# Optimization experiments

Hardware: AMD Instinct MI355X
Metric: run time of the kernel (lower is better)

The kernel has to match this reference:

```python
import jax, jax.numpy as jnp
import numpy as np

B, C, H, W = 32, 256, 32, 32
HID, NPATH = 128, 4


def setup_inputs() -> dict:
    key = jax.random.key(0)
    ks = jax.random.split(key, 16)
    s = lambda *sh: 1.0 / np.sqrt(sh[-1])
    inp = {
        "lidar": jax.random.normal(ks[0], (B, C, H, W), jnp.float32),
        "hsi": jax.random.normal(ks[1], (B, C, H, W), jnp.float32),
        "x": jax.random.normal(ks[2], (B, C, H, W), jnp.float32),
        # shared Cross_Self_attention params
        "Wq": jax.random.normal(ks[3], (C, C), jnp.float32) * s(C, C),
        "bq": jnp.zeros((C,), jnp.float32),
        "Wk": jax.random.normal(ks[4], (C, C), jnp.float32) * s(C, C),
        "bk": jnp.zeros((C,), jnp.float32),
        "Wv": jax.random.normal(ks[5], (C, C), jnp.float32) * s(C, C),
        "bv": jnp.zeros((C,), jnp.float32),
        # 1x1 conv: [out=C, in=2C]
        "conv_w": jax.random.normal(ks[6], (C, 2 * C), jnp.float32) * s(C, 2 * C),
        "conv_b": jnp.zeros((C,), jnp.float32),
        # router MLP
        "r_w1": jax.random.normal(ks[7], (HID, 2 * C), jnp.float32) * s(HID, 2 * C),
        "r_b1": jnp.zeros((HID,), jnp.float32),
        "r_w2": jax.random.normal(ks[8], (NPATH, HID), jnp.float32) * s(NPATH, HID),
        "r_b2": jnp.zeros((NPATH,), jnp.float32),
    }
    return inp


def _cross_self_attn(xq, yv, Wq, bq, Wk, bk, Wv, bv):
    # xq, yv: [b, s, c]
    q = xq @ Wq.T + bq
    k = xq @ Wk.T + bk
    v = yv @ Wv.T + bv
    probs = jax.nn.softmax(jnp.einsum("bsc,btc->bst", q, k), axis=-1)  # [b,s,s]
    return jnp.einsum("bst,btc->bsc", probs, q * v)  # bilinear value Q*V


def reference(lidar, hsi, x, Wq, bq, Wk, bk, Wv, bv, conv_w, conv_b, r_w1, r_b1, r_w2, r_b2):
    b, c, h, w = lidar.shape
    # Router: concat channels, spatial mean pool, MLP, sigmoid
    g = jnp.concatenate([lidar, hsi], axis=1).mean(axis=(2, 3))  # [b, 2c]
    path_prob = jax.nn.sigmoid(jax.nn.relu(g @ r_w1.T + r_b1) @ r_w2.T + r_b2)

    l = lidar.reshape(b, c, h * w).transpose(0, 2, 1)  # b (h w) c
    hh = hsi.reshape(b, c, h * w).transpose(0, 2, 1)

    h_emb = _cross_self_attn(l, hh, Wq, bq, Wk, bk, Wv, bv)  # [b, hw, c]
    l_emb = _cross_self_attn(hh, l, Wq, bq, Wk, bk, Wv, bv)

    h_emb = h_emb.transpose(0, 2, 1).reshape(b, c, h, w)
    l_emb = l_emb.transpose(0, 2, 1).reshape(b, c, h, w)

    cat = jnp.concatenate([l_emb, h_emb], axis=1)  # [b, 2c, h, w]
    emb = jnp.einsum("bihw,oi->bohw", cat, conv_w) + conv_b[None, :, None, None] + x
    return emb, path_prob
```

## Files before the change

### kernel.cpp

```cpp
#include <hip/hip_runtime.h>
#include <stdint.h>

typedef unsigned short u16;
typedef unsigned int u32;
typedef _Float16 f16;
typedef _Float16 f16x8 __attribute__((ext_vector_type(8)));
typedef _Float16 f16x4 __attribute__((ext_vector_type(4)));
typedef float f32x4 __attribute__((ext_vector_type(4)));

#define B_ 32
#define C_ 256
#define S_ 1024

__global__ __launch_bounds__(256) void k_mlp(
    const float* __restrict__ g,
    const float* __restrict__ w1, const float* __restrict__ b1,
    const float* __restrict__ w2, const float* __restrict__ b2,
    float* __restrict__ out)
{
    int b = blockIdx.x, tid = threadIdx.x;
    __shared__ float sg[512];
    __shared__ float sh[128];
    sg[tid]     = g[b*512 + tid]       * (1.0f/1024.0f);
    sg[tid+256] = g[b*512 + 256 + tid] * (1.0f/1024.0f);
    __syncthreads();
    if (tid < 128){
        float a = b1[tid];
        const float* w = w1 + (size_t)tid*512;
        #pragma unroll 4
        for (int k = 0; k < 512; k += 4){
            float4 wv = *(const float4*)(w + k);
            a += sg[k]*wv.x + sg[k+1]*wv.y + sg[k+2]*wv.z + sg[k+3]*wv.w;
        }
        sh[tid] = fmaxf(a, 0.f);
    }
    __syncthreads();
    if (tid < 4){
        float a = b2[tid];
        const float* w = w2 + (size_t)tid*128;
        for (int k = 0; k < 128; ++k) a += sh[k]*w[k];
        out[(size_t)8388608 + b*4 + tid] = 1.f/(1.f+expf(-a));
    }
}

__global__ __launch_bounds__(256) void k_cvtw(
    const float* __restrict__ Wq, const float* __restrict__ Wk,
    const float* __restrict__ Wv, const float* __restrict__ cw,
    f16* __restrict__ Wqf, f16* __restrict__ Wkf,
    f16* __restrict__ Wvf, f16* __restrict__ cwf)
{
    int i = (blockIdx.x*256 + threadIdx.x) * 4;
    const float* src; f16* dst; int off;
    if (i < 65536){ src = Wq; dst = Wqf; off = i; }
    else if (i < 131072){ src = Wk; dst = Wkf; off = i - 65536; }
    else if (i < 196608){ src = Wv; dst = Wvf; off = i - 131072; }
    else { src = cw; dst = cwf; off = i - 196608; }
    float4 v = *(const float4*)(src + off);
    f16x4 r = { (f16)v.x, (f16)v.y, (f16)v.z, (f16)v.w };
    *(f16x4*)(dst + off) = r;
}

__global__ __launch_bounds__(256) void k_cvt(
    const float* __restrict__ lidar, const float* __restrict__ hsi,
    f16* __restrict__ lidT, f16* __restrict__ hsiT,
    float* __restrict__ g)
{
    int z = blockIdx.z, which = z >> 5, b = z & 31;
    const float* src = (which ? hsi : lidar) + (size_t)b*C_*S_;
    f16* dst = (which ? hsiT : lidT) + (size_t)b*S_*C_;
    int tid = threadIdx.x;
    int c4 = blockIdx.y*64 + (tid&15)*4;
    int s4 = blockIdx.x*64 + (tid>>4)*4;
    float4 m[4];
    #pragma unroll
    for (int r = 0; r < 4; ++r) m[r] = *(const float4*)(src + (size_t)(c4+r)*S_ + s4);
    f16x4 t0 = { (f16)m[0].x, (f16)m[1].x, (f16)m[2].x, (f16)m[3].x };
    f16x4 t1 = { (f16)m[0].y, (f16)m[1].y, (f16)m[2].y, (f16)m[3].y };
    f16x4 t2 = { (f16)m[0].z, (f16)m[1].z, (f16)m[2].z, (f16)m[3].z };
    f16x4 t3 = { (f16)m[0].w, (f16)m[1].w, (f16)m[2].w, (f16)m[3].w };
    *(f16x4*)(dst + (size_t)(s4+0)*C_ + c4) = t0;
    *(f16x4*)(dst + (size_t)(s4+1)*C_ + c4) = t1;
    *(f16x4*)(dst + (size_t)(s4+2)*C_ + c4) = t2;
    *(f16x4*)(dst + (size_t)(s4+3)*C_ + c4) = t3;
    float ps[4];
    #pragma unroll
    for (int r = 0; r < 4; ++r){
        ps[r] = m[r].x + m[r].y + m[r].z + m[r].w;
        ps[r] += __shfl_xor(ps[r], 16, 64);
        ps[r] += __shfl_xor(ps[r], 32, 64);
    }
    __shared__ float sred[4][64];
    int wv = tid>>6, lane = tid&63;
    if ((lane>>4) == 0){
        #pragma unroll
        for (int r = 0; r < 4; ++r) sred[wv][(lane&15)*4 + r] = ps[r];
    }
    __syncthreads();
    if (tid < 64){
        float v = sred[0][tid] + sred[1][tid] + sred[2][tid] + sred[3][tid];
        atomicAdd(&g[b*512 + which*256 + blockIdx.y*64 + tid], v);
    }
}

__global__ __launch_bounds__(256) void k_qkv(
    const f16* __restrict__ lidT, const f16* __restrict__ hsiT,
    const f16* __restrict__ Wqf, const f16* __restrict__ Wkf, const f16* __restrict__ Wvf,
    const float* __restrict__ bq, const float* __restrict__ bk, const float* __restrict__ bv,
    f16* __restrict__ Qf_l, f16* __restrict__ Kf_l,
    f16* __restrict__ Qf_h, f16* __restrict__ Kf_h,
    f16* __restrict__ Qt_l, f16* __restrict__ Qt_h,
    f16* __restrict__ Vt_l, f16* __restrict__ Vt_h)
{
    int z = blockIdx.z, combo = z >> 5, b = z & 31, ww = combo % 3;
    const f16* In = ((combo < 3) ? lidT : hsiT) + (size_t)b*S_*C_;
    const f16* Wf = (ww==0) ? Wqf : (ww==1) ? Wkf : Wvf;
    const float* bias = (ww==0) ? bq : (ww==1) ? bk : bv;
    int s0 = blockIdx.x*64, o0 = blockIdx.y*64;
    int tid = threadIdx.x, w = tid>>6, lane = tid&63, quad = lane>>4, l15 = lane&15;

    __shared__ __align__(16) f16 sA[64*72];
    __shared__ __align__(16) f16 sB[64*72];

    f32x4 D[4];
    #pragma unroll
    for (int i = 0; i < 4; ++i) D[i] = (f32x4){0.f,0.f,0.f,0.f};

    int row = tid>>2, c16 = (tid&3)*16;
    for (int c0 = 0; c0 < 256; c0 += 64){
        __syncthreads();
        *(f16x8*)&sA[row*72 + c16]     = *(const f16x8*)(In + (size_t)(s0+row)*C_ + c0 + c16);
        *(f16x8*)&sA[row*72 + c16 + 8] = *(const f16x8*)(In + (size_t)(s0+row)*C_ + c0 + c16 + 8);
        *(f16x8*)&sB[row*72 + c16]     = *(const f16x8*)(Wf + (size_t)(o0+row)*C_ + c0 + c16);
        *(f16x8*)&sB[row*72 + c16 + 8] = *(const f16x8*)(Wf + (size_t)(o0+row)*C_ + c0 + c16 + 8);
        __syncthreads();
        #pragma unroll
        for (int sub = 0; sub < 2; ++sub){
            f16x8 a = *(const f16x8*)&sA[(w*16+l15)*72 + sub*32 + quad*8];
            #pragma unroll
            for (int bt = 0; bt < 4; ++bt){
                f16x8 bb = *(const f16x8*)&sB[(bt*16+l15)*72 + sub*32 + quad*8];
                D[bt] = __builtin_amdgcn_mfma_f32_16x16x32_f16(a, bb, D[bt], 0,0,0);
            }
        }
    }
    float bi[4];
    #pragma unroll
    for (int bt = 0; bt < 4; ++bt) bi[bt] = bias[o0 + bt*16 + l15];

    if (ww == 0){
        f16* F = ((combo==0) ? Qf_l : Qf_h) + (size_t)b*S_*C_;
        #pragma unroll
        for (int bt = 0; bt < 4; ++bt)
            #pragma unroll
            for (int r = 0; r < 4; ++r)
                F[(size_t)(s0 + w*16 + quad*4 + r)*C_ + o0 + bt*16 + l15] = (f16)(D[bt][r] + bi[bt]);
    } else if (ww == 1){
        f16* F = ((combo==1) ? Kf_l : Kf_h) + (size_t)b*S_*C_;
        #pragma unroll
        for (int bt = 0; bt < 4; ++bt)
            #pragma unroll
            for (int r = 0; r < 4; ++r)
                F[(size_t)(s0 + w*16 + quad*4 + r)*C_ + o0 + bt*16 + l15] = (f16)(D[bt][r] + bi[bt]);
    }
    if (ww != 1){
        __syncthreads();
        #pragma unroll
        for (int bt = 0; bt < 4; ++bt)
            #pragma unroll
            for (int r = 0; r < 4; ++r)
                sA[(bt*16+l15)*72 + w*16 + quad*4 + r] = (f16)(D[bt][r] + bi[bt]);
        __syncthreads();
        f16* T = (combo==0) ? Qt_l : (combo==3) ? Qt_h : (combo==2) ? Vt_l : Vt_h;
        T += (size_t)b*C_*S_;
        int o_r = tid>>2, s16b = (tid&3)*16;
        *(f16x8*)(T + (size_t)(o0+o_r)*S_ + s0 + s16b)     = *(const f16x8*)&sA[o_r*72 + s16b];
        *(f16x8*)(T + (size_t)(o0+o_r)*S_ + s0 + s16b + 8) = *(const f16x8*)&sA[o_r*72 + s16b + 8];
    }
}

__global__ __launch_bounds__(256) void k_qv(
    const f16* __restrict__ Qt_l, const f16* __restrict__ Qt_h,
    const f16* __restrict__ Vt_l, const f16* __restrict__ Vt_h,
    f16* __restrict__ QVT1, f16* __restrict__ QVT2)
{
    size_t idx = (size_t)(blockIdx.x*256 + threadIdx.x) * 8;
    f16x8 a = *(const f16x8*)(Qt_l+idx);
    f16x8 b = *(const f16x8*)(Vt_h+idx);
    *(f16x8*)(QVT1+idx) = a*b;
    f16x8 c = *(const f16x8*)(Qt_h+idx);
    f16x8 d = *(const f16x8*)(Vt_l+idx);
    *(f16x8*)(QVT2+idx) = c*d;
}

__global__ __launch_bounds__(256, 2) void k_attn(
    const f16* __restrict__ Qf_l, const f16* __restrict__ Kf_l,
    const f16* __restrict__ Qf_h, const f16* __restrict__ Kf_h,
    const f16* __restrict__ QVT1, const f16* __restrict__ QVT2,
    f16* __restrict__ cat)
{
    int inst = blockIdx.y;
    int b = inst >> 1, which = inst & 1;
    const f16* Qf  = (which ? Qf_h : Qf_l) + (size_t)b*S_*C_;
    const f16* Kf  = (which ? Kf_h : Kf_l) + (size_t)b*S_*C_;
    const f16* QVT = (which ? QVT2 : QVT1) + (size_t)b*C_*S_;
    f16* outp = cat + (size_t)b*S_*512 + (which ? 0 : 256);
    int s0 = blockIdx.x*64;
    int tid = threadIdx.x, w = tid>>6, lane = tid&63, quad = lane>>4, l15 = lane&15;

    __shared__ __align__(16) f16 sK[64*264];
    __shared__ __align__(16) f16 sV[256*72];
    __shared__ __align__(16) f16 sPw[4][16*66];

    f16x8 qa[8];
    {
        const f16* qrow = Qf + (size_t)(s0 + w*16 + l15)*C_ + quad*8;
        #pragma unroll
        for (int i = 0; i < 8; ++i) qa[i] = *(const f16x8*)(qrow + i*32);
    }
    float mrun[4], lpart[4];
    #pragma unroll
    for (int r = 0; r < 4; ++r){ mrun[r] = -1e30f; lpart[r] = 0.f; }
    f32x4 pacc[16];
    #pragma unroll
    for (int i = 0; i < 16; ++i) pacc[i] = (f32x4){0.f,0.f,0.f,0.f};

    f16x8 kreg[8], vreg[8];
    #pragma unroll
    for (int p = 0; p < 8; ++p){
        int idx = p*256 + tid;
        kreg[p] = *(const f16x8*)(Kf + (size_t)(idx>>5)*C_ + (idx&31)*8);
        vreg[p] = *(const f16x8*)(QVT + (size_t)(idx>>3)*S_ + (idx&7)*8);
    }

    for (int tt = 0; tt < 16; ++tt){
        __syncthreads();
        #pragma unroll
        for (int p = 0; p < 8; ++p){
            int idx = p*256 + tid;
            *(f16x8*)&sK[(idx>>5)*264 + (idx&31)*8] = kreg[p];
            *(f16x8*)&sV[(idx>>3)*72  + (idx&7)*8]  = vreg[p];
        }
        __syncthreads();

        if (tt < 15){
            int t0n = (tt+1)*64;
            #pragma unroll
            for (int p = 0; p < 8; ++p){
                int idx = p*256 + tid;
                kreg[p] = *(const f16x8*)(Kf + (size_t)(t0n + (idx>>5))*C_ + (idx&31)*8);
                vreg[p] = *(const f16x8*)(QVT + (size_t)(idx>>3)*S_ + t0n + (idx&7)*8);
            }
        }

        f32x4 sacc[4];
        #pragma unroll
        for (int bt = 0; bt < 4; ++bt) sacc[bt] = (f32x4){0.f,0.f,0.f,0.f};
        __builtin_amdgcn_s_setprio(1);
        #pragma unroll
        for (int ks = 0; ks < 8; ++ks){
            #pragma unroll
            for (int bt = 0; bt < 4; ++bt){
                f16x8 kb = *(const f16x8*)&sK[(bt*16+l15)*264 + ks*32 + quad*8];
                sacc[bt] = __builtin_amdgcn_mfma_f32_16x16x32_f16(qa[ks], kb, sacc[bt], 0,0,0);
            }
        }
        __builtin_amdgcn_s_setprio(0);

        float tm[4];
        #pragma unroll
        for (int r = 0; r < 4; ++r){
            float t = fmaxf(fmaxf(sacc[0][r], sacc[1][r]), fmaxf(sacc[2][r], sacc[3][r]));
            #pragma unroll
            for (int off = 1; off < 16; off <<= 1) t = fmaxf(t, __shfl_xor(t, off, 64));
            tm[r] = t;
        }
        bool need = (tm[0] > mrun[0]+8.f) | (tm[1] > mrun[1]+8.f) |
                    (tm[2] > mrun[2]+8.f) | (tm[3] > mrun[3]+8.f);
        if (__any(need)){
            #pragma unroll
            for (int r = 0; r < 4; ++r){
                float mn = fmaxf(mrun[r], tm[r]);
                float al = __expf(mrun[r] - mn);
                mrun[r] = mn;
                lpart[r] *= al;
                #pragma unroll
                for (int cf = 0; cf < 16; ++cf) pacc[cf][r] *= al;
            }
        }
        #pragma unroll
        for (int r = 0; r < 4; ++r){
            float local = 0.f;
            #pragma unroll
            for (int bt = 0; bt < 4; ++bt){
                float p = __expf(sacc[bt][r] - mrun[r]);
                sPw[w][(quad*4+r)*66 + bt*16 + l15] = (f16)p;
                local += p;
            }
            lpart[r] += local;
        }
        f16x8 pa0 = *(const f16x8*)&sPw[w][l15*66 + quad*8];
        f16x8 pa1 = *(const f16x8*)&sPw[w][l15*66 + 32 + quad*8];

        __builtin_amdgcn_s_setprio(1);
        #pragma unroll
        for (int cf = 0; cf < 16; ++cf){
            f16x8 vb0 = *(const f16x8*)&sV[(cf*16+l15)*72 + quad*8];
            f16x8 vb1 = *(const f16x8*)&sV[(cf*16+l15)*72 + 32 + quad*8];
            pacc[cf] = __builtin_amdgcn_mfma_f32_16x16x32_f16(pa0, vb0, pacc[cf], 0,0,0);
            pacc[cf] = __builtin_amdgcn_mfma_f32_16x16x32_f16(pa1, vb1, pacc[cf], 0,0,0);
        }
        __builtin_amdgcn_s_setprio(0);
    }

    #pragma unroll
    for (int r = 0; r < 4; ++r){
        #pragma unroll
        for (int off = 1; off < 16; off <<= 1) lpart[r] += __shfl_xor(lpart[r], off, 64);
    }
    #pragma unroll
    for (int r = 0; r < 4; ++r){
        int s = w*16 + quad*4 + r;
        float rl = 1.f / lpart[r];
        #pragma unroll
        for (int cf = 0; cf < 16; ++cf)
            outp[(size_t)(s0+s)*512 + cf*16 + l15] = (f16)(pacc[cf][r] * rl);
    }
}

__global__ __launch_bounds__(256) void k_conv(
    const f16* __restrict__ cat, const f16* __restrict__ cwf,
    const float* __restrict__ cb, const float* __restrict__ x,
    float* __restrict__ out)
{
    int b = blockIdx.z;
    int s0 = blockIdx.x*64, o0 = blockIdx.y*64;
    int tid = threadIdx.x, w = tid>>6, lane = tid&63, quad = lane>>4, l15 = lane&15;

    __shared__ __align__(16) f16 sA[64*72];
    __shared__ __align__(16) f16 sB[64*72];

    f32x4 D[4];
    #pragma unroll
    for (int i = 0; i < 4; ++i) D[i] = (f32x4){0.f,0.f,0.f,0.f};

    const f16* catb = cat + (size_t)b*S_*512;
    int row = tid>>2, c16 = (tid&3)*16;
    for (int i0 = 0; i0 < 512; i0 += 64){
        __syncthreads();
        *(f16x8*)&sA[row*72 + c16]     = *(const f16x8*)(cwf + (size_t)(o0+row)*512 + i0 + c16);
        *(f16x8*)&sA[row*72 + c16 + 8] = *(const f16x8*)(cwf + (size_t)(o0+row)*512 + i0 + c16 + 8);
        *(f16x8*)&sB[row*72 + c16]     = *(const f16x8*)(catb + (size_t)(s0+row)*512 + i0 + c16);
        *(f16x8*)&sB[row*72 + c16 + 8] = *(const f16x8*)(catb + (size_t)(s0+row)*512 + i0 + c16 + 8);
        __syncthreads();
        #pragma unroll
        for (int sub = 0; sub < 2; ++sub){
            f16x8 a = *(const f16x8*)&sA[(w*16+l15)*72 + sub*32 + quad*8];
            #pragma unroll
            for (int bt = 0; bt < 4; ++bt){
                f16x8 bb = *(const f16x8*)&sB[(bt*16+l15)*72 + sub*32 + quad*8];
                D[bt] = __builtin_amdgcn_mfma_f32_16x16x32_f16(a, bb, D[bt], 0,0,0);
            }
        }
    }
    #pragma unroll
    for (int r = 0; r < 4; ++r){
        int o_loc = w*16 + quad*4 + r;
        float cbv = cb[o0 + o_loc];
        size_t base = (size_t)b*C_*S_ + (size_t)(o0+o_loc)*S_ + s0;
        #pragma unroll
        for (int bt = 0; bt < 4; ++bt){
            size_t a = base + bt*16 + l15;
            out[a] = D[bt][r] + cbv + x[a];
        }
    }
}

extern "C" void kernel_launch(void* const* d_in, const int* in_sizes, int n_in,
                              void* d_out, int out_size, void* d_ws, size_t ws_size,
                              hipStream_t stream)
{
    const float* lidar = (const float*)d_in[0];
    const float* hsi   = (const float*)d_in[1];
    const float* x     = (const float*)d_in[2];
    const float* Wq = (const float*)d_in[3];  const float* bq = (const float*)d_in[4];
    const float* Wk = (const float*)d_in[5];  const float* bk = (const float*)d_in[6];
    const float* Wv = (const float*)d_in[7];  const float* bv = (const float*)d_in[8];
    const float* cw = (const float*)d_in[9];  const float* cb = (const float*)d_in[10];
    const float* rw1 = (const float*)d_in[11]; const float* rb1 = (const float*)d_in[12];
    const float* rw2 = (const float*)d_in[13]; const float* rb2 = (const float*)d_in[14];
    float* outF = (float*)d_out;
    char* ws = (char*)d_ws;
    const size_t M = 1ull<<20;

    f16* lidT = (f16*)(ws +   0*M);
    f16* hsiT = (f16*)(ws +  16*M);
    f16* Qf_l = (f16*)(ws +  32*M);
    f16* Kf_l = (f16*)(ws +  48*M);
    f16* Qf_h = (f16*)(ws +  64*M);
    f16* Kf_h = (f16*)(ws +  80*M);
    f16* Qt_l = (f16*)(ws +  96*M);
    f16* Qt_h = (f16*)(ws + 112*M);
    f16* cat  = (f16*)(ws + 128*M);
    float* g  = (float*)(ws + 160*M);
    f16* Wqf  = (f16*)(ws + 161*M);
    f16* Wkf  = (f16*)(ws + 161*M + 131072);
    f16* Wvf  = (f16*)(ws + 161*M + 262144);
    f16* cwf  = (f16*)(ws + 161*M + 393216);
    f16* QVT1 = lidT;
    f16* QVT2 = hsiT;
    f16* Vt_l = (f16*)d_out;
    f16* Vt_h = (f16*)d_out + 8388608;

    hipMemsetAsync(g, 0, 4096*sizeof(float), stream);
    k_cvtw<<<320, 256, 0, stream>>>(Wq, Wk, Wv, cw, Wqf, Wkf, Wvf, cwf);
    k_cvt<<<dim3(16,4,64), 256, 0, stream>>>(lidar, hsi, lidT, hsiT, g);
    k_mlp<<<32, 256, 0, stream>>>(g, rw1, rb1, rw2, rb2, outF);
    k_qkv<<<dim3(16,4,192), 256, 0, stream>>>(lidT, hsiT, Wqf, Wkf, Wvf, bq, bk, bv,
                                              Qf_l, Kf_l, Qf_h, Kf_h, Qt_l, Qt_h, Vt_l, Vt_h);
    k_qv<<<4096, 256, 0, stream>>>(Qt_l, Qt_h, Vt_l, Vt_h, QVT1, QVT2);
    k_attn<<<dim3(16,64), 256, 0, stream>>>(Qf_l, Kf_l, Qf_h, Kf_h, QVT1, QVT2, cat);
    k_conv<<<dim3(16,4,32), 256, 0, stream>>>(cat, cwf, cb, x, outF);
}
```

Baseline: 400.9 us.

## Process two query tiles per attention block to reuse K/V shared tiles

Each attention block now handles 128 query rows (two 64-row groups per wave) instead of 64, so every K and QV tile staged in shared memory feeds twice as many MFMAs. This halves the block count and the total global K/V traffic. The register-prefetch double buffering of the next K/V tile is removed, and loads now go straight from global to shared memory between barriers. Register pressure roughly doubles for the accumulators (pacc now holds 32 f32x4 per thread), which risks spills or lower occupancy under launch_bounds(256,2). Load latency is also no longer hidden by prefetch.

```diff
diff --git a/kernel.cpp b/kernel.cpp
--- a/kernel.cpp
+++ b/kernel.cpp
@@ -204,126 +204,133 @@
     const f16* Kf  = (which ? Kf_h : Kf_l) + (size_t)b*S_*C_;
     const f16* QVT = (which ? QVT2 : QVT1) + (size_t)b*C_*S_;
     f16* outp = cat + (size_t)b*S_*512 + (which ? 0 : 256);
-    int s0 = blockIdx.x*64;
+    int s0 = blockIdx.x*128;
     int tid = threadIdx.x, w = tid>>6, lane = tid&63, quad = lane>>4, l15 = lane&15;
 
     __shared__ __align__(16) f16 sK[64*264];
     __shared__ __align__(16) f16 sV[256*72];
     __shared__ __align__(16) f16 sPw[4][16*66];
 
-    f16x8 qa[8];
-    {
-        const f16* qrow = Qf + (size_t)(s0 + w*16 + l15)*C_ + quad*8;
-        #pragma unroll
-        for (int i = 0; i < 8; ++i) qa[i] = *(const f16x8*)(qrow + i*32);
-    }
-    float mrun[4], lpart[4];
-    #pragma unroll
-    for (int r = 0; r < 4; ++r){ mrun[r] = -1e30f; lpart[r] = 0.f; }
-    f32x4 pacc[16];
-    #pragma unroll
-    for (int i = 0; i < 16; ++i) pacc[i] = (f32x4){0.f,0.f,0.f,0.f};
-
-    f16x8 kreg[8], vreg[8];
-    #pragma unroll
-    for (int p = 0; p < 8; ++p){
-        int idx = p*256 + tid;
-        kreg[p] = *(const f16x8*)(Kf + (size_t)(idx>>5)*C_ + (idx&31)*8);
-        vreg[p] = *(const f16x8*)(QVT + (size_t)(idx>>3)*S_ + (idx&7)*8);
-    }
+    f16x8 qa[2][8];
+    #pragma unroll
+    for (int g = 0; g < 2; ++g){
+        const f16* qrow = Qf + (size_t)(s0 + g*64 + w*16 + l15)*C_ + quad*8;
+        #pragma unroll
+        for (int i = 0; i < 8; ++i) qa[g][i] = *(const f16x8*)(qrow + i*32);
+    }
+    float mrun[2][4], lpart[2][4];
+    #pragma unroll
+    for (int g = 0; g < 2; ++g)
+        #pragma unroll
+        for (int r = 0; r < 4; ++r){ mrun[g][r] = -1e30f; lpart[g][r] = 0.f; }
+    f32x4 pacc[2][16];
+    #pragma unroll
+    for (int g = 0; g < 2; ++g)
+        #pragma unroll
+        for (int i = 0; i < 16; ++i) pacc[g][i] = (f32x4){0.f,0.f,0.f,0.f};
 
     for (int tt = 0; tt < 16; ++tt){
+        int t0 = tt*64;
         __syncthreads();
         #pragma unroll
         for (int p = 0; p < 8; ++p){
             int idx = p*256 + tid;
-            *(f16x8*)&sK[(idx>>5)*264 + (idx&31)*8] = kreg[p];
-            *(f16x8*)&sV[(idx>>3)*72  + (idx&7)*8]  = vreg[p];
-        }
-        __syncthreads();
-
-        if (tt < 15){
-            int t0n = (tt+1)*64;
-            #pragma unroll
-            for (int p = 0; p < 8; ++p){
-                int idx = p*256 + tid;
-                kreg[p] = *(const f16x8*)(Kf + (size_t)(t0n + (idx>>5))*C_ + (idx&31)*8);
-                vreg[p] = *(const f16x8*)(QVT + (size_t)(idx>>3)*S_ + t0n + (idx&7)*8);
-            }
-        }
-
-        f32x4 sacc[4];
-        #pragma unroll
-        for (int bt = 0; bt < 4; ++bt) sacc[bt] = (f32x4){0.f,0.f,0.f,0.f};
+            int row = idx >> 5, c8 = (idx & 31)*8;
+            *(f16x8*)&sK[row*264 + c8] = *(const f16x8*)(Kf + (size_t)(t0+row)*C_ + c8);
+        }
+        #pragma unroll
+        for (int p = 0; p < 8; ++p){
+            int idx = p*256 + tid;
+            int row = idx >> 3, t8 = (idx & 7)*8;
+            *(f16x8*)&sV[row*72 + t8] = *(const f16x8*)(QVT + (size_t)row*S_ + t0 + t8);
+        }
+        __syncthreads();
+
+        f32x4 sacc[2][4];
+        #pragma unroll
+        for (int g = 0; g < 2; ++g)
+            #pragma unroll
+            for (int bt = 0; bt < 4; ++bt) sacc[g][bt] = (f32x4){0.f,0.f,0.f,0.f};
         __builtin_amdgcn_s_setprio(1);
         #pragma unroll
         for (int ks = 0; ks < 8; ++ks){
             #pragma unroll
             for (int bt = 0; bt < 4; ++bt){
                 f16x8 kb = *(const f16x8*)&sK[(bt*16+l15)*264 + ks*32 + quad*8];
-                sacc[bt] = __builtin_amdgcn_mfma_f32_16x16x32_f16(qa[ks], kb, sacc[bt], 0,0,0);
+                sacc[0][bt] = __builtin_amdgcn_mfma_f32_16x16x32_f16(qa[0][ks], kb, sacc[0][bt], 0,0,0);
+                sacc[1][bt] = __builtin_amdgcn_mfma_f32_16x16x32_f16(qa[1][ks], kb, sacc[1][bt], 0,0,0);
             }
         }
         __builtin_amdgcn_s_setprio(0);
 
-        float tm[4];
-        #pragma unroll
-        for (int r = 0; r < 4; ++r){
-            float t = fmaxf(fmaxf(sacc[0][r], sacc[1][r]), fmaxf(sacc[2][r], sacc[3][r]));
-            #pragma unroll
-            for (int off = 1; off < 16; off <<= 1) t = fmaxf(t, __shfl_xor(t, off, 64));
-            tm[r] = t;
-        }
-        bool need = (tm[0] > mrun[0]+8.f) | (tm[1] > mrun[1]+8.f) |
-                    (tm[2] > mrun[2]+8.f) | (tm[3] > mrun[3]+8.f);
-        if (__any(need)){
+        f16x8 pa[2][2];
+        #pragma unroll
+        for (int g = 0; g < 2; ++g){
+            float tm[4];
             #pragma unroll
             for (int r = 0; r < 4; ++r){
-                float mn = fmaxf(mrun[r], tm[r]);
-                float al = __expf(mrun[r] - mn);
-                mrun[r] = mn;
-                lpart[r] *= al;
+                float t = fmaxf(fmaxf(sacc[g][0][r], sacc[g][1][r]),
+                                fmaxf(sacc[g][2][r], sacc[g][3][r]));
                 #pragma unroll
-                for (int cf = 0; cf < 16; ++cf) pacc[cf][r] *= al;
-            }
-        }
-        #pragma unroll
-        for (int r = 0; r < 4; ++r){
-            float local = 0.f;
-            #pragma unroll
-            for (int bt = 0; bt < 4; ++bt){
-                float p = __expf(sacc[bt][r] - mrun[r]);
-                sPw[w][(quad*4+r)*66 + bt*16 + l15] = (f16)p;
-                local += p;
-            }
-            lpart[r] += local;
-        }
-        f16x8 pa0 = *(const f16x8*)&sPw[w][l15*66 + quad*8];
-        f16x8 pa1 = *(const f16x8*)&sPw[w][l15*66 + 32 + quad*8];
+                for (int off = 1; off < 16; off <<= 1) t = fmaxf(t, __shfl_xor(t, off, 64));
+                tm[r] = t;
+            }
+            bool need = (tm[0] > mrun[g][0]+8.f) | (tm[1] > mrun[g][1]+8.f) |
+                        (tm[2] > mrun[g][2]+8.f) | (tm[3] > mrun[g][3]+8.f);
+            if (__any(need)){
+                #pragma unroll
+                for (int r = 0; r < 4; ++r){
+                    float mn = fmaxf(mrun[g][r], tm[r]);
+                    float al = __expf(mrun[g][r] - mn);
+                    mrun[g][r] = mn;
+                    lpart[g][r] *= al;
+                    #pragma unroll
+                    for (int cf = 0; cf < 16; ++cf) pacc[g][cf][r] *= al;
+                }
+            }
+            #pragma unroll
+            for (int r = 0; r < 4; ++r){
+                float local = 0.f;
+                #pragma unroll
+                for (int bt = 0; bt < 4; ++bt){
+                    float p = __expf(sacc[g][bt][r] - mrun[g][r]);
+                    sPw[w][(quad*4+r)*66 + bt*16 + l15] = (f16)p;
+                    local += p;
+                }
+                lpart[g][r] += local;
+            }
+            pa[g][0] = *(const f16x8*)&sPw[w][l15*66 + quad*8];
+            pa[g][1] = *(const f16x8*)&sPw[w][l15*66 + 32 + quad*8];
+        }
 
         __builtin_amdgcn_s_setprio(1);
         #pragma unroll
         for (int cf = 0; cf < 16; ++cf){
             f16x8 vb0 = *(const f16x8*)&sV[(cf*16+l15)*72 + quad*8];
             f16x8 vb1 = *(const f16x8*)&sV[(cf*16+l15)*72 + 32 + quad*8];
-            pacc[cf] = __builtin_amdgcn_mfma_f32_16x16x32_f16(pa0, vb0, pacc[cf], 0,0,0);
-            pacc[cf] = __builtin_amdgcn_mfma_f32_16x16x32_f16(pa1, vb1, pacc[cf], 0,0,0);
+            pacc[0][cf] = __builtin_amdgcn_mfma_f32_16x16x32_f16(pa[0][0], vb0, pacc[0][cf], 0,0,0);
+            pacc[0][cf] = __builtin_amdgcn_mfma_f32_16x16x32_f16(pa[0][1], vb1, pacc[0][cf], 0,0,0);
+            pacc[1][cf] = __builtin_amdgcn_mfma_f32_16x16x32_f16(pa[1][0], vb0, pacc[1][cf], 0,0,0);
+            pacc[1][cf] = __builtin_amdgcn_mfma_f32_16x16x32_f16(pa[1][1], vb1, pacc[1][cf], 0,0,0);
         }
         __builtin_amdgcn_s_setprio(0);
     }
 
     #pragma unroll
-    for (int r = 0; r < 4; ++r){
-        #pragma unroll
-        for (int off = 1; off < 16; off <<= 1) lpart[r] += __shfl_xor(lpart[r], off, 64);
-    }
-    #pragma unroll
-    for (int r = 0; r < 4; ++r){
-        int s = w*16 + quad*4 + r;
-        float rl = 1.f / lpart[r];
-        #pragma unroll
-        for (int cf = 0; cf < 16; ++cf)
-            outp[(size_t)(s0+s)*512 + cf*16 + l15] = (f16)(pacc[cf][r] * rl);
+    for (int g = 0; g < 2; ++g){
+        #pragma unroll
+        for (int r = 0; r < 4; ++r){
+            #pragma unroll
+            for (int off = 1; off < 16; off <<= 1) lpart[g][r] += __shfl_xor(lpart[g][r], off, 64);
+        }
+        #pragma unroll
+        for (int r = 0; r < 4; ++r){
+            int s = g*64 + w*16 + quad*4 + r;
+            float rl = 1.f / lpart[g][r];
+            #pragma unroll
+            for (int cf = 0; cf < 16; ++cf)
+                outp[(size_t)(s0+s)*512 + cf*16 + l15] = (f16)(pacc[g][cf][r] * rl);
+        }
     }
 }
 
@@ -418,6 +425,6 @@
     k_qkv<<<dim3(16,4,192), 256, 0, stream>>>(lidT, hsiT, Wqf, Wkf, Wvf, bq, bk, bv,
                                               Qf_l, Kf_l, Qf_h, Kf_h, Qt_l, Qt_h, Vt_l, Vt_h);
     k_qv<<<4096, 256, 0, stream>>>(Qt_l, Qt_h, Vt_l, Vt_h, QVT1, QVT2);
-    k_attn<<<dim3(16,64), 256, 0, stream>>>(Qf_l, Kf_l, Qf_h, Kf_h, QVT1, QVT2, cat);
+    k_attn<<<dim3(8,64), 256, 0, stream>>>(Qf_l, Kf_l, Qf_h, Kf_h, QVT1, QVT2, cat);
     k_conv<<<dim3(16,4,32), 256, 0, stream>>>(cat, cwf, cb, x, outF);
 }
```

New measurement: 490.0 us. 1.22x slower.

## Widen QKV and conv GEMM tiles to cover all 256 output channels per block

Applied to the files above, without the earlier changes.

The QKV projection and 1x1 conv kernels now compute all 256 output channels per block instead of a 64-wide slice, so each input/cat tile is loaded from global memory once rather than four times. Each block stages the full weight K-slice (256x64) in shared memory and keeps 16 MFMA accumulators per wave. The conv kernel swaps operand roles so its stores along the spatial dimension are more contiguous. In exchange, shared memory and register use per block rise and the grid shrinks fourfold, which can lower occupancy.

```diff
diff --git a/kernel.cpp b/kernel.cpp
--- a/kernel.cpp
+++ b/kernel.cpp
@@ -111,70 +111,72 @@
     f16* __restrict__ Qt_l, f16* __restrict__ Qt_h,
     f16* __restrict__ Vt_l, f16* __restrict__ Vt_h)
 {
-    int z = blockIdx.z, combo = z >> 5, b = z & 31, ww = combo % 3;
+    int z = blockIdx.y, combo = z >> 5, b = z & 31, ww = combo % 3;
     const f16* In = ((combo < 3) ? lidT : hsiT) + (size_t)b*S_*C_;
     const f16* Wf = (ww==0) ? Wqf : (ww==1) ? Wkf : Wvf;
     const float* bias = (ww==0) ? bq : (ww==1) ? bk : bv;
-    int s0 = blockIdx.x*64, o0 = blockIdx.y*64;
+    int s0 = blockIdx.x*64;
     int tid = threadIdx.x, w = tid>>6, lane = tid&63, quad = lane>>4, l15 = lane&15;
 
-    __shared__ __align__(16) f16 sA[64*72];
-    __shared__ __align__(16) f16 sB[64*72];
-
-    f32x4 D[4];
-    #pragma unroll
-    for (int i = 0; i < 4; ++i) D[i] = (f32x4){0.f,0.f,0.f,0.f};
-
-    int row = tid>>2, c16 = (tid&3)*16;
+    __shared__ __align__(16) f16 sIn[64*72];
+    __shared__ __align__(16) f16 sW[256*72];
+
+    f32x4 D[16];
+    #pragma unroll
+    for (int i = 0; i < 16; ++i) D[i] = (f32x4){0.f,0.f,0.f,0.f};
+
+    int row2 = tid>>2, c16 = (tid&3)*16;
     for (int c0 = 0; c0 < 256; c0 += 64){
         __syncthreads();
-        *(f16x8*)&sA[row*72 + c16]     = *(const f16x8*)(In + (size_t)(s0+row)*C_ + c0 + c16);
-        *(f16x8*)&sA[row*72 + c16 + 8] = *(const f16x8*)(In + (size_t)(s0+row)*C_ + c0 + c16 + 8);
-        *(f16x8*)&sB[row*72 + c16]     = *(const f16x8*)(Wf + (size_t)(o0+row)*C_ + c0 + c16);
-        *(f16x8*)&sB[row*72 + c16 + 8] = *(const f16x8*)(Wf + (size_t)(o0+row)*C_ + c0 + c16 + 8);
+        *(f16x8*)&sIn[row2*72 + c16]     = *(const f16x8*)(In + (size_t)(s0+row2)*C_ + c0 + c16);
+        *(f16x8*)&sIn[row2*72 + c16 + 8] = *(const f16x8*)(In + (size_t)(s0+row2)*C_ + c0 + c16 + 8);
+        #pragma unroll
+        for (int p = 0; p < 8; ++p){
+            int idx = p*256 + tid;
+            int row = idx >> 3, c8 = (idx & 7)*8;
+            *(f16x8*)&sW[row*72 + c8] = *(const f16x8*)(Wf + (size_t)row*C_ + c0 + c8);
+        }
         __syncthreads();
         #pragma unroll
         for (int sub = 0; sub < 2; ++sub){
-            f16x8 a = *(const f16x8*)&sA[(w*16+l15)*72 + sub*32 + quad*8];
-            #pragma unroll
-            for (int bt = 0; bt < 4; ++bt){
-                f16x8 bb = *(const f16x8*)&sB[(bt*16+l15)*72 + sub*32 + quad*8];
-                D[bt] = __builtin_amdgcn_mfma_f32_16x16x32_f16(a, bb, D[bt], 0,0,0);
-            }
-        }
-    }
-    float bi[4];
-    #pragma unroll
-    for (int bt = 0; bt < 4; ++bt) bi[bt] = bias[o0 + bt*16 + l15];
-
-    if (ww == 0){
-        f16* F = ((combo==0) ? Qf_l : Qf_h) + (size_t)b*S_*C_;
-        #pragma unroll
-        for (int bt = 0; bt < 4; ++bt)
+            f16x8 a = *(const f16x8*)&sIn[(w*16+l15)*72 + sub*32 + quad*8];
+            #pragma unroll
+            for (int ot = 0; ot < 16; ++ot){
+                f16x8 bb = *(const f16x8*)&sW[(ot*16+l15)*72 + sub*32 + quad*8];
+                D[ot] = __builtin_amdgcn_mfma_f32_16x16x32_f16(a, bb, D[ot], 0,0,0);
+            }
+        }
+    }
+    float bi[16];
+    #pragma unroll
+    for (int ot = 0; ot < 16; ++ot) bi[ot] = bias[ot*16 + l15];
+
+    if (ww != 2){
+        f16* F = (ww==0) ? ((combo==0) ? Qf_l : Qf_h) : ((combo==1) ? Kf_l : Kf_h);
+        F += (size_t)b*S_*C_;
+        #pragma unroll
+        for (int ot = 0; ot < 16; ++ot)
             #pragma unroll
             for (int r = 0; r < 4; ++r)
-                F[(size_t)(s0 + w*16 + quad*4 + r)*C_ + o0 + bt*16 + l15] = (f16)(D[bt][r] + bi[bt]);
-    } else if (ww == 1){
-        f16* F = ((combo==1) ? Kf_l : Kf_h) + (size_t)b*S_*C_;
-        #pragma unroll
-        for (int bt = 0; bt < 4; ++bt)
+                F[(size_t)(s0 + w*16 + quad*4 + r)*C_ + ot*16 + l15] = (f16)(D[ot][r] + bi[ot]);
+    }
+    if (ww != 1){
+        __syncthreads();
+        #pragma unroll
+        for (int ot = 0; ot < 16; ++ot)
             #pragma unroll
             for (int r = 0; r < 4; ++r)
-                F[(size_t)(s0 + w*16 + quad*4 + r)*C_ + o0 + bt*16 + l15] = (f16)(D[bt][r] + bi[bt]);
-    }
-    if (ww != 1){
-        __syncthreads();
-        #pragma unroll
-        for (int bt = 0; bt < 4; ++bt)
-            #pragma unroll
-            for (int r = 0; r < 4; ++r)
-                sA[(bt*16+l15)*72 + w*16 + quad*4 + r] = (f16)(D[bt][r] + bi[bt]);
+                sW[(ot*16+l15)*72 + w*16 + quad*4 + r] = (f16)(D[ot][r] + bi[ot]);
         __syncthreads();
         f16* T = (combo==0) ? Qt_l : (combo==3) ? Qt_h : (combo==2) ? Vt_l : Vt_h;
         T += (size_t)b*C_*S_;
         int o_r = tid>>2, s16b = (tid&3)*16;
-        *(f16x8*)(T + (size_t)(o0+o_r)*S_ + s0 + s16b)     = *(const f16x8*)&sA[o_r*72 + s16b];
-        *(f16x8*)(T + (size_t)(o0+o_r)*S_ + s0 + s16b + 8) = *(const f16x8*)&sA[o_r*72 + s16b + 8];
+        #pragma unroll
+        for (int rep = 0; rep < 4; ++rep){
+            int orow = rep*64 + o_r;
+            *(f16x8*)(T + (size_t)orow*S_ + s0 + s16b)     = *(const f16x8*)&sW[orow*72 + s16b];
+            *(f16x8*)(T + (size_t)orow*S_ + s0 + s16b + 8) = *(const f16x8*)&sW[orow*72 + s16b + 8];
+        }
     }
 }
 
@@ -332,45 +334,48 @@
     const float* __restrict__ cb, const float* __restrict__ x,
     float* __restrict__ out)
 {
-    int b = blockIdx.z;
-    int s0 = blockIdx.x*64, o0 = blockIdx.y*64;
+    int b = blockIdx.y;
+    int s0 = blockIdx.x*64;
     int tid = threadIdx.x, w = tid>>6, lane = tid&63, quad = lane>>4, l15 = lane&15;
 
-    __shared__ __align__(16) f16 sA[64*72];
-    __shared__ __align__(16) f16 sB[64*72];
-
-    f32x4 D[4];
-    #pragma unroll
-    for (int i = 0; i < 4; ++i) D[i] = (f32x4){0.f,0.f,0.f,0.f};
+    __shared__ __align__(16) f16 sCat[64*72];
+    __shared__ __align__(16) f16 sW[256*72];
+
+    f32x4 D[16];
+    #pragma unroll
+    for (int i = 0; i < 16; ++i) D[i] = (f32x4){0.f,0.f,0.f,0.f};
 
     const f16* catb = cat + (size_t)b*S_*512;
-    int row = tid>>2, c16 = (tid&3)*16;
+    int row2 = tid>>2, c16 = (tid&3)*16;
     for (int i0 = 0; i0 < 512; i0 += 64){
         __syncthreads();
-        *(f16x8*)&sA[row*72 + c16]     = *(const f16x8*)(cwf + (size_t)(o0+row)*512 + i0 + c16);
-        *(f16x8*)&sA[row*72 + c16 + 8] = *(const f16x8*)(cwf + (size_t)(o0+row)*512 + i0 + c16 + 8);
-        *(f16x8*)&sB[row*72 + c16]     = *(const f16x8*)(catb + (size_t)(s0+row)*512 + i0 + c16);
-        *(f16x8*)&sB[row*72 + c16 + 8] = *(const f16x8*)(catb + (size_t)(s0+row)*512 + i0 + c16 + 8);
+        *(f16x8*)&sCat[row2*72 + c16]     = *(const f16x8*)(catb + (size_t)(s0+row2)*512 + i0 + c16);
+        *(f16x8*)&sCat[row2*72 + c16 + 8] = *(const f16x8*)(catb + (size_t)(s0+row2)*512 + i0 + c16 + 8);
+        #pragma unroll
+        for (int p = 0; p < 8; ++p){
+            int idx = p*256 + tid;
+            int row = idx >> 3, c8 = (idx & 7)*8;
+            *(f16x8*)&sW[row*72 + c8] = *(const f16x8*)(cwf + (size_t)row*512 + i0 + c8);
+        }
         __syncthreads();
         #pragma unroll
         for (int sub = 0; sub < 2; ++sub){
-            f16x8 a = *(const f16x8*)&sA[(w*16+l15)*72 + sub*32 + quad*8];
-            #pragma unroll
-            for (int bt = 0; bt < 4; ++bt){
-                f16x8 bb = *(const f16x8*)&sB[(bt*16+l15)*72 + sub*32 + quad*8];
-                D[bt] = __builtin_amdgcn_mfma_f32_16x16x32_f16(a, bb, D[bt], 0,0,0);
-            }
-        }
-    }
-    #pragma unroll
-    for (int r = 0; r < 4; ++r){
-        int o_loc = w*16 + quad*4 + r;
-        float cbv = cb[o0 + o_loc];
-        size_t base = (size_t)b*C_*S_ + (size_t)(o0+o_loc)*S_ + s0;
-        #pragma unroll
-        for (int bt = 0; bt < 4; ++bt){
-            size_t a = base + bt*16 + l15;
-            out[a] = D[bt][r] + cbv + x[a];
+            f16x8 bcat = *(const f16x8*)&sCat[(w*16+l15)*72 + sub*32 + quad*8];
+            #pragma unroll
+            for (int ot = 0; ot < 16; ++ot){
+                f16x8 aw = *(const f16x8*)&sW[(ot*16+l15)*72 + sub*32 + quad*8];
+                D[ot] = __builtin_amdgcn_mfma_f32_16x16x32_f16(aw, bcat, D[ot], 0,0,0);
+            }
+        }
+    }
+    #pragma unroll
+    for (int ot = 0; ot < 16; ++ot){
+        #pragma unroll
+        for (int r = 0; r < 4; ++r){
+            int o = ot*16 + quad*4 + r;
+            float cbv = cb[o];
+            size_t a = (size_t)b*C_*S_ + (size_t)o*S_ + s0 + w*16 + l15;
+            out[a] = D[ot][r] + cbv + x[a];
         }
     }
 }
@@ -415,9 +420,9 @@
     k_cvtw<<<320, 256, 0, stream>>>(Wq, Wk, Wv, cw, Wqf, Wkf, Wvf, cwf);
     k_cvt<<<dim3(16,4,64), 256, 0, stream>>>(lidar, hsi, lidT, hsiT, g);
     k_mlp<<<32, 256, 0, stream>>>(g, rw1, rb1, rw2, rb2, outF);
-    k_qkv<<<dim3(16,4,192), 256, 0, stream>>>(lidT, hsiT, Wqf, Wkf, Wvf, bq, bk, bv,
-                                              Qf_l, Kf_l, Qf_h, Kf_h, Qt_l, Qt_h, Vt_l, Vt_h);
+    k_qkv<<<dim3(16,192), 256, 0, stream>>>(lidT, hsiT, Wqf, Wkf, Wvf, bq, bk, bv,
+                                            Qf_l, Kf_l, Qf_h, Kf_h, Qt_l, Qt_h, Vt_l, Vt_h);
     k_qv<<<4096, 256, 0, stream>>>(Qt_l, Qt_h, Vt_l, Vt_h, QVT1, QVT2);
     k_attn<<<dim3(16,64), 256, 0, stream>>>(Qf_l, Kf_l, Qf_h, Kf_h, QVT1, QVT2, cat);
-    k_conv<<<dim3(16,4,32), 256, 0, stream>>>(cat, cwf, cb, x, outF);
-}
+    k_conv<<<dim3(16,32), 256, 0, stream>>>(cat, cwf, cb, x, outF);
+}
```

After: 413.3 us. 1.03x slower.
